# Optimization experiments

Hardware: AMD Instinct MI355X
Metric: run time of the kernel (lower is better)

Reference implementation:

```python
import jax, jax.numpy as jnp
from jax import lax
import numpy as np

H, HKV, D = 16, 4, 128          # query heads, kv heads, head dim
ROT_DIM = 128                    # rotary applied to full head dim
BASE = 10000.0


def rope_cos_sin(S, dtype):
    inv_freq = 1.0 / (BASE ** (jnp.arange(0, ROT_DIM, 2, dtype=jnp.float32) / ROT_DIM))
    t = jnp.arange(S, dtype=jnp.float32)
    freqs = jnp.outer(t, inv_freq)          # (S, ROT_DIM//2)
    return jnp.cos(freqs).astype(dtype), jnp.sin(freqs).astype(dtype)


def apply_rope(x, cos, sin):
    # x: (B, S, h, D); non-interleaved (GPT-NeoX) halves
    d2 = ROT_DIM // 2
    x1, x2 = x[..., :d2], x[..., d2:ROT_DIM]
    c = cos[None, :, None, :]
    s = sin[None, :, None, :]
    rot = jnp.concatenate([x1 * c - x2 * s, x2 * c + x1 * s], axis=-1)
    if ROT_DIM < x.shape[-1]:
        rot = jnp.concatenate([rot, x[..., ROT_DIM:]], axis=-1)
    return rot


def setup_inputs() -> dict:
    key = jax.random.key(0)
    ks = jax.random.split(key, 7)
    B, S, E = 2, 2048, 2048
    qkv_dim = D * (H + 2 * HKV)  # 3072
    return {
        "x": jax.random.normal(ks[0], (B, S, E), jnp.float32),
        "w_in": jax.random.normal(ks[1], (qkv_dim, E), jnp.float32) * (1.0 / np.sqrt(E)),
        "b_in": jax.random.normal(ks[2], (qkv_dim,), jnp.float32) * 0.02,
        "conv_w": jax.random.normal(ks[3], (qkv_dim, 1, 4), jnp.float32) * 0.5,
        "conv_b": jax.random.normal(ks[4], (qkv_dim,), jnp.float32) * 0.02,
        "w_out": jax.random.normal(ks[5], (E, H * D), jnp.float32) * (1.0 / np.sqrt(H * D)),
        "b_out": jax.random.normal(ks[6], (E,), jnp.float32) * 0.02,
    }


def reference(x, w_in, b_in, conv_w, conv_b, w_out, b_out):
    B, S, E = x.shape
    K = conv_w.shape[-1]
    # fused QKV projection
    qkv = x @ w_in.T + b_in                                  # (B, S, 3072)
    # causal depthwise conv1d (torch conv with padding=K-1 then keep first S)
    lhs = jnp.pad(qkv.transpose(0, 2, 1), ((0, 0), (0, 0), (K - 1, 0)))  # (B, C, S+K-1)
    conv = lax.conv_general_dilated(
        lhs, conv_w, (1,), "VALID",
        dimension_numbers=("NCH", "OIH", "NCH"),
        feature_group_count=conv_w.shape[0],
    )
    qkv = (conv + conv_b[None, :, None]).transpose(0, 2, 1)  # (B, S, 3072)
    # split q / kv (GQA)
    q = qkv[..., : H * D].reshape(B, S, H, D)
    kv = qkv[..., H * D :].reshape(B, S, 2, HKV, D)
    cos, sin = rope_cos_sin(S, x.dtype)
    q = apply_rope(q, cos, sin)
    k = apply_rope(kv[:, :, 0], cos, sin)
    v = kv[:, :, 1]
    rep = H // HKV
    k = jnp.repeat(k, rep, axis=2)                           # (B, S, H, D)
    v = jnp.repeat(v, rep, axis=2)
    scale = 1.0 / np.sqrt(D)  # softmax_scale=None -> 1/sqrt(head_dim)
    scores = jnp.einsum("bshd,bthd->bhst", q, k) * scale     # (B, H, S, S)
    causal_mask = jnp.tril(jnp.ones((S, S), bool))
    scores = jnp.where(causal_mask[None, None], scores, jnp.finfo(scores.dtype).min)
    attn = jax.nn.softmax(scores, axis=-1)
    ctx = jnp.einsum("bhst,bthd->bshd", attn, v).reshape(B, S, H * D)
    return ctx @ w_out.T + b_out
```

## Files before the change

### kernel.cpp

```cpp
#include <hip/hip_runtime.h>
#include <type_traits>

#define S_LEN 2048
#define BATCH 2
#define EDIM  2048
#define NH    16
#define NKV   4
#define HDIM  128
#define QKVD  3072
#define QSCALE 0.12751579107188777f

typedef __attribute__((ext_vector_type(8))) short short8;
typedef __attribute__((ext_vector_type(4))) float f32x4;

__device__ __forceinline__ ushort f2bf(float f) {
  union { float f; unsigned u; } un; un.f = f;
  unsigned u = un.u + 0x7fffu + ((un.u >> 16) & 1u);
  return (ushort)(u >> 16);
}
__device__ __forceinline__ float bf2f(ushort h) {
  union { unsigned u; float f; } un; un.u = ((unsigned)h) << 16;
  return un.f;
}
__device__ __forceinline__ unsigned cvt_pk_bf16(float lo, float hi) {
  unsigned r;
  asm("v_cvt_pk_bf16_f32 %0, %1, %2" : "=v"(r) : "v"(lo), "v"(hi));
  return r;
}
__device__ __forceinline__ float fexp2(float x) { return __builtin_amdgcn_exp2f(x); }

__device__ __forceinline__ void load_lds16(const void* g, void* l) {
  __builtin_amdgcn_global_load_lds((const __attribute__((address_space(1))) void*)g,
                                   (__attribute__((address_space(3))) void*)l,
                                   16, 0, 0);
}

__global__ __launch_bounds__(256) void cast3(const float* __restrict__ a,
                                             const float* __restrict__ b,
                                             const float* __restrict__ c,
                                             ushort* __restrict__ oa,
                                             ushort* __restrict__ ob,
                                             ushort* __restrict__ oc) {
  int i = blockIdx.x * 256 + threadIdx.x;
  const float* s; ushort* d; int j;
  if (i < 2097152)      { s = a; d = oa; j = i; }
  else if (i < 3670016) { s = b; d = ob; j = i - 2097152; }
  else                  { s = c; d = oc; j = i - 3670016; }
  float4 v = ((const float4*)s)[j];
  ushort4 o;
  o.x = f2bf(v.x); o.y = f2bf(v.y); o.z = f2bf(v.z); o.w = f2bf(v.w);
  ((ushort4*)d)[j] = o;
}

__global__ __launch_bounds__(256) void transpose_cw(const float* __restrict__ cw,
                                                    float* __restrict__ cwT) {
  int i = blockIdx.x * 256 + threadIdx.x;
  int c = i >> 2, j = i & 3;
  cwT[j * QKVD + c] = cw[i];
}

__global__ __launch_bounds__(256) void rope_table(float* __restrict__ cosT,
                                                  float* __restrict__ sinT) {
  int i = blockIdx.x * 256 + threadIdx.x;
  int s = i >> 6, d = i & 63;
  float inv = expf(-(float)d * 0.14391156831212787f);
  float f = (float)s * inv;
  float sv, cv;
  sincosf(f, &sv, &cv);
  cosT[i] = cv;
  sinT[i] = sv;
}

template <bool OBF>
__global__ __launch_bounds__(256) void gemm_bt(
    const ushort* __restrict__ A, const ushort* __restrict__ Bt,
    const float* __restrict__ bias, void* __restrict__ Cv,
    int M, int N, int K) {
  __shared__ __align__(16) ushort As[128 * 32];
  __shared__ __align__(16) ushort Bs[128 * 32];
  const int tid = threadIdx.x;
  const int wid = tid >> 6, lane = tid & 63;
  const int l15 = lane & 15, lg = lane >> 4;
  const int nTn = N >> 7;
  const int cpx = gridDim.x >> 3;
  const int swz = ((int)blockIdx.x & 7) * cpx + ((int)blockIdx.x >> 3);
  const int m0 = (swz / nTn) * 128, n0 = (swz % nTn) * 128;
  const int wr = (wid >> 1) * 64, wc = (wid & 1) * 64;
  f32x4 acc[4][4] = {};

  for (int k0 = 0; k0 < K; k0 += 32) {
#pragma unroll
    for (int j = 0; j < 2; ++j) {
      const int c = j * 256 + wid * 64 + lane;
      load_lds16(A + (size_t)(m0 + (c >> 2)) * K + k0 + (c & 3) * 8,
                 As + (j * 256 + wid * 64) * 8);
      load_lds16(Bt + (size_t)(n0 + (c >> 2)) * K + k0 + (c & 3) * 8,
                 Bs + (j * 256 + wid * 64) * 8);
    }
    __syncthreads();
    short8 af[4], bf[4];
#pragma unroll
    for (int i = 0; i < 4; i++) {
      af[i] = *(const short8*)&As[(wr + i * 16 + l15) * 32 + lg * 8];
      bf[i] = *(const short8*)&Bs[(wc + i * 16 + l15) * 32 + lg * 8];
    }
#pragma unroll
    for (int mi = 0; mi < 4; mi++)
#pragma unroll
      for (int ni = 0; ni < 4; ni++)
        acc[mi][ni] = __builtin_amdgcn_mfma_f32_16x16x32_bf16(af[mi], bf[ni], acc[mi][ni], 0, 0, 0);
    __syncthreads();
  }

#pragma unroll
  for (int mi = 0; mi < 4; mi++) {
#pragma unroll
    for (int ni = 0; ni < 4; ni++) {
      const int col = n0 + wc + ni * 16 + l15;
      const float bv = bias[col];
#pragma unroll
      for (int r = 0; r < 4; r++) {
        const int row = m0 + wr + mi * 16 + lg * 4 + r;
        if constexpr (OBF)
          ((ushort*)Cv)[(size_t)row * N + col] = f2bf(acc[mi][ni][r] + bv);
        else
          ((float*)Cv)[(size_t)row * N + col] = acc[mi][ni][r] + bv;
      }
    }
  }
}

template <bool OBF>
__global__ __launch_bounds__(512, 2) void gemm256(
    const ushort* __restrict__ A, const ushort* __restrict__ Bt,
    const float* __restrict__ bias, void* __restrict__ Cv,
    int M, int N, int K) {
  __shared__ __align__(16) ushort LA[4][8192];
  __shared__ __align__(16) ushort LB[4][8192];
  const int tid = threadIdx.x;
  const int wid = tid >> 6, lane = tid & 63;
  const int l15 = lane & 15, lg = lane >> 4;
  const int wr = wid >> 2, wc = wid & 3;
  const int nTn = N >> 8;
  const int cpx = gridDim.x >> 3;
  const int swz = ((int)blockIdx.x & 7) * cpx + ((int)blockIdx.x >> 3);
  const int m0 = (swz / nTn) * 256, n0 = (swz % nTn) * 256;
  const ushort* Ag = A + (size_t)m0 * K;
  const ushort* Bg = Bt + (size_t)n0 * K;
  const int coff = (lg ^ ((l15 >> 1) & 3)) * 8;
  const int abase = (wr * 128 + l15) * 32 + coff;
  const int bbase = (wc * 64 + l15) * 32 + coff;
  const int nk = K >> 5;

  f32x4 acc[8][4] = {};

  auto stage_one = [&](const ushort* G, ushort* Ls, int k0) {
#pragma unroll
    for (int i = 0; i < 2; ++i) {
      const int c = i * 512 + tid;
      const int row = c >> 2, cc = c & 3;
      const int scc = cc ^ ((row >> 1) & 3);
      load_lds16(G + (size_t)row * K + k0 + scc * 8,
                 Ls + (i * 512 + wid * 64) * 8);
    }
  };

#pragma unroll
  for (int t = 0; t < 3; ++t) {
    stage_one(Ag, LA[t], t * 32);
    stage_one(Bg, LB[t], t * 32);
  }
  asm volatile("s_waitcnt vmcnt(8)" ::: "memory");
  __builtin_amdgcn_s_barrier();

  auto ktile = [&](auto VMC, auto STG, int t) {
    constexpr int VM = decltype(VMC)::value;
    constexpr bool STAGE = decltype(STG)::value;
    const int slot = t & 3;
    const ushort* Las = LA[slot];
    const ushort* Lbs = LB[slot];
    short8 afr[8], bfr[4];
#pragma unroll
    for (int n = 0; n < 4; ++n) bfr[n] = *(const short8*)&Lbs[bbase + n * 512];
#pragma unroll
    for (int m = 0; m < 8; ++m) afr[m] = *(const short8*)&Las[abase + m * 512];
    if constexpr (STAGE) {
      stage_one(Ag, LA[(t + 3) & 3], (t + 3) * 32);
      stage_one(Bg, LB[(t + 3) & 3], (t + 3) * 32);
    }
    __builtin_amdgcn_s_barrier();
    __builtin_amdgcn_s_setprio(1);
#pragma unroll
    for (int m = 0; m < 8; ++m)
#pragma unroll
      for (int n = 0; n < 4; ++n)
        acc[m][n] = __builtin_amdgcn_mfma_f32_16x16x32_bf16(afr[m], bfr[n], acc[m][n], 0, 0, 0);
    __builtin_amdgcn_s_setprio(0);
    if constexpr (VM == 8)      asm volatile("s_waitcnt vmcnt(8)" ::: "memory");
    else if constexpr (VM == 4) asm volatile("s_waitcnt vmcnt(4)" ::: "memory");
    else if constexpr (VM == 0) asm volatile("s_waitcnt vmcnt(0)" ::: "memory");
    __builtin_amdgcn_s_barrier();
  };

  using tru = std::integral_constant<bool, true>;
  using fal = std::integral_constant<bool, false>;
  for (int t = 0; t + 3 < nk; ++t)
    ktile(std::integral_constant<int, 8>{}, tru{}, t);
  ktile(std::integral_constant<int, 4>{}, fal{}, nk - 3);
  ktile(std::integral_constant<int, 0>{}, fal{}, nk - 2);
  ktile(std::integral_constant<int, -1>{}, fal{}, nk - 1);

#pragma unroll
  for (int m = 0; m < 8; ++m)
#pragma unroll
    for (int n = 0; n < 4; ++n) {
      const int col = n0 + wc * 64 + n * 16 + l15;
      const float bv = bias[col];
#pragma unroll
      for (int r = 0; r < 4; ++r) {
        const int row = m0 + wr * 128 + m * 16 + lg * 4 + r;
        if constexpr (OBF)
          ((ushort*)Cv)[(size_t)row * N + col] = f2bf(acc[m][n][r] + bv);
        else
          ((float*)Cv)[(size_t)row * N + col] = acc[m][n][r] + bv;
      }
    }
}

__global__ __launch_bounds__(256) void conv_rope(
    const ushort* __restrict__ qkv, const float* __restrict__ cwT,
    const float* __restrict__ cb, const float* __restrict__ cosT,
    const float* __restrict__ sinT, ushort* __restrict__ Qo,
    ushort* __restrict__ Ko, ushort* __restrict__ Vo) {
  const int token = blockIdx.x;
  const int s = token & (S_LEN - 1);
  const int p = blockIdx.y * 256 + threadIdx.x;

  auto conv4 = [&](int c0, float out[4]) {
    const float4 bb = *(const float4*)&cb[c0];
    out[0] = bb.x; out[1] = bb.y; out[2] = bb.z; out[3] = bb.w;
#pragma unroll
    for (int j = 0; j < 4; j++) {
      int ss = s - 3 + j;
      if (ss >= 0) {
        ushort4 v = *(const ushort4*)&qkv[(size_t)(token - 3 + j) * QKVD + c0];
        const float4 w = *(const float4*)&cwT[j * QKVD + c0];
        out[0] += bf2f(v.x) * w.x;
        out[1] += bf2f(v.y) * w.y;
        out[2] += bf2f(v.z) * w.z;
        out[3] += bf2f(v.w) * w.w;
      }
    }
  };

  if (p < 256) {
    const int h = p >> 4, d0 = (p & 15) * 4;
    const int c1 = h * 128 + d0;
    float x1[4], x2[4];
    conv4(c1, x1); conv4(c1 + 64, x2);
    const float4 co = *(const float4*)&cosT[s * 64 + d0];
    const float4 si = *(const float4*)&sinT[s * 64 + d0];
    ushort4 o1, o2v;
    o1.x = f2bf((x1[0] * co.x - x2[0] * si.x) * QSCALE);
    o1.y = f2bf((x1[1] * co.y - x2[1] * si.y) * QSCALE);
    o1.z = f2bf((x1[2] * co.z - x2[2] * si.z) * QSCALE);
    o1.w = f2bf((x1[3] * co.w - x2[3] * si.w) * QSCALE);
    o2v.x = f2bf((x2[0] * co.x + x1[0] * si.x) * QSCALE);
    o2v.y = f2bf((x2[1] * co.y + x1[1] * si.y) * QSCALE);
    o2v.z = f2bf((x2[2] * co.z + x1[2] * si.z) * QSCALE);
    o2v.w = f2bf((x2[3] * co.w + x1[3] * si.w) * QSCALE);
    const size_t base = ((size_t)token * NH + h) * HDIM + d0;
    *(ushort4*)&Qo[base] = o1;
    *(ushort4*)&Qo[base + 64] = o2v;
  } else if (p < 320) {
    const int idx = p - 256, h = idx >> 4, d0 = (idx & 15) * 4;
    const int c1 = 2048 + h * 128 + d0;
    float x1[4], x2[4];
    conv4(c1, x1); conv4(c1 + 64, x2);
    const float4 co = *(const float4*)&cosT[s * 64 + d0];
    const float4 si = *(const float4*)&sinT[s * 64 + d0];
    ushort4 o1, o2v;
    o1.x = f2bf(x1[0] * co.x - x2[0] * si.x);
    o1.y = f2bf(x1[1] * co.y - x2[1] * si.y);
    o1.z = f2bf(x1[2] * co.z - x2[2] * si.z);
    o1.w = f2bf(x1[3] * co.w - x2[3] * si.w);
    o2v.x = f2bf(x2[0] * co.x + x1[0] * si.x);
    o2v.y = f2bf(x2[1] * co.y + x1[1] * si.y);
    o2v.z = f2bf(x2[2] * co.z + x1[2] * si.z);
    o2v.w = f2bf(x2[3] * co.w + x1[3] * si.w);
    const size_t base = ((size_t)token * NKV + h) * HDIM + d0;
    *(ushort4*)&Ko[base] = o1;
    *(ushort4*)&Ko[base + 64] = o2v;
  } else if (p < 448) {
    const int idx = p - 320;
    const int c0 = 2560 + idx * 4;
    float v[4];
    conv4(c0, v);
    const int hd = idx * 4;
    const int h = hd >> 7, d = hd & 127;
    ushort4 o;
    o.x = f2bf(v[0]); o.y = f2bf(v[1]); o.z = f2bf(v[2]); o.w = f2bf(v[3]);
    *(ushort4*)&Vo[((size_t)token * NKV + h) * HDIM + d] = o;
  }
}

__global__ __launch_bounds__(256) void transpose_v(const ushort* __restrict__ Vb,
                                                   ushort* __restrict__ Vt) {
  __shared__ ushort t[64][65];
  const int tid = threadIdx.x;
  const int s0 = blockIdx.x * 64, d0 = blockIdx.y * 64;
  const int g = blockIdx.z;
  const int b = g >> 2, kvh = g & 3;
#pragma unroll
  for (int p = 0; p < 8; p++) {
    int idx = p * 256 + tid;
    int r = idx >> 5, c2 = (idx & 31) * 2;
    ushort2 v = *(const ushort2*)&Vb[((size_t)(b * S_LEN + s0 + r) * NKV + kvh) * HDIM + d0 + c2];
    t[r][c2] = v.x; t[r][c2 + 1] = v.y;
  }
  __syncthreads();
#pragma unroll
  for (int p = 0; p < 8; p++) {
    int idx = p * 256 + tid;
    int dr = idx >> 5, sc2 = (idx & 31) * 2;
    ushort2 v; v.x = t[sc2][dr]; v.y = t[sc2 + 1][dr];
    *(ushort2*)&Vt[((size_t)g * HDIM + d0 + dr) * S_LEN + s0 + sc2] = v;
  }
}

__global__ __launch_bounds__(256, 2) void attn(
    const ushort* __restrict__ Q, const ushort* __restrict__ K,
    const ushort* __restrict__ Vt, ushort* __restrict__ ctx) {
  __shared__ __align__(16) ushort Ks[2][64 * 128];
  __shared__ __align__(16) ushort Vs[2][128 * 64];
  const int tid = threadIdx.x;
  const int wid = tid >> 6, lane = tid & 63;
  const int l15 = lane & 15, lg = lane >> 4;
  const int bkv = blockIdx.x;
  const int b = bkv >> 2, kvh = bkv & 3;
  const int h = kvh * 4 + wid;
  const int qb = (gridDim.y - 1) - blockIdx.y;
  const int q0 = qb * 16;

  const ushort* Kbase  = K  + ((size_t)b * S_LEN * NKV + kvh) * HDIM;
  const ushort* Vtbase = Vt + (size_t)bkv * HDIM * S_LEN;

  short8 qf[4];
#pragma unroll
  for (int kd = 0; kd < 4; kd++)
    qf[kd] = *(const short8*)&Q[(((size_t)(b * S_LEN + q0 + l15)) * NH + h) * HDIM + kd * 32 + lg * 8];

  auto stage = [&](int tile, int bufi) {
    const int j0t = tile * 64;
#pragma unroll
    for (int p = 0; p < 4; ++p) {
      const int i = wid * 4 + p;
      {
        const int row = i * 4 + (lane >> 4);
        const int cs  = (lane & 15) ^ (row & 7);
        load_lds16(Kbase + (size_t)(j0t + row) * (NKV * HDIM) + cs * 8,
                   &Ks[bufi][i * 512]);
      }
      {
        const int d  = i * 8 + (lane >> 3);
        const int cs = (lane & 7) ^ (d & 7);
        load_lds16(Vtbase + (size_t)d * S_LEN + j0t + cs * 8,
                   &Vs[bufi][i * 512]);
      }
    }
  };

  f32x4 o2[8] = {};
  float m_run = -3e30f, l_run = 0.f;
  const int ntile = q0 / 64 + 1;
  const int qrow = q0 + l15;

  stage(0, 0);
  __syncthreads();
  int buf = 0;
  for (int jt = 0; jt < ntile; ++jt) {
    const int j0 = jt * 64;
    if (jt + 1 < ntile) stage(jt + 1, buf ^ 1);

    f32x4 sa[4] = {};
#pragma unroll
    for (int t = 0; t < 4; ++t) {
      const int r = t * 16 + l15;
#pragma unroll
      for (int kd = 0; kd < 4; ++kd) {
        short8 kf = *(const short8*)&Ks[buf][r * 128 + (((kd * 4 + lg) ^ (r & 7)) * 8)];
        sa[t] = __builtin_amdgcn_mfma_f32_16x16x32_bf16(kf, qf[kd], sa[t], 0, 0, 0);
      }
    }

    float pv[4][4];
    float mx = -3e30f;
#pragma unroll
    for (int t = 0; t < 4; ++t)
#pragma unroll
      for (int r = 0; r < 4; ++r) {
        float v = sa[t][r];
        if (j0 + t * 16 + lg * 4 + r > qrow) v = -3e30f;
        pv[t][r] = v;
        mx = fmaxf(mx, v);
      }
    mx = fmaxf(mx, __shfl_xor(mx, 16));
    mx = fmaxf(mx, __shfl_xor(mx, 32));
    const float mnew = fmaxf(m_run, mx);
    float sum = 0.f;
#pragma unroll
    for (int t = 0; t < 4; ++t)
#pragma unroll
      for (int r = 0; r < 4; ++r) {
        float p = fexp2(pv[t][r] - mnew);
        pv[t][r] = p;
        sum += p;
      }
    sum += __shfl_xor(sum, 16);
    sum += __shfl_xor(sum, 32);
    const float fac = fexp2(m_run - mnew);
    m_run = mnew;
    l_run = l_run * fac + sum;
#pragma unroll
    for (int dt = 0; dt < 8; ++dt)
#pragma unroll
      for (int r = 0; r < 4; ++r) o2[dt][r] *= fac;

    unsigned pk[4][2];
#pragma unroll
    for (int t = 0; t < 4; ++t)
#pragma unroll
      for (int p = 0; p < 2; ++p)
        pk[t][p] = cvt_pk_bf16(pv[t][2 * p], pv[t][2 * p + 1]);

    union U8 { unsigned u[4]; short8 s; } pfk[2];
#pragma unroll
    for (int ks = 0; ks < 2; ++ks)
#pragma unroll
      for (int j = 0; j < 4; ++j) {
        const int src = ((lg & 1) * 2 + (j >> 1)) * 16 + l15;
        unsigned v0 = __shfl((int)pk[ks * 2][j & 1], src);
        unsigned v1 = __shfl((int)pk[ks * 2 + 1][j & 1], src);
        pfk[ks].u[j] = (lg >= 2) ? v1 : v0;
      }

#pragma unroll
    for (int dt = 0; dt < 8; ++dt) {
      const int d = dt * 16 + l15;
#pragma unroll
      for (int ks = 0; ks < 2; ++ks) {
        short8 vf = *(const short8*)&Vs[buf][d * 64 + (((ks * 4 + lg) ^ (d & 7)) * 8)];
        o2[dt] = __builtin_amdgcn_mfma_f32_16x16x32_bf16(vf, pfk[ks].s, o2[dt], 0, 0, 0);
      }
    }

    __syncthreads();
    buf ^= 1;
  }

  const float inv_l = 1.f / l_run;
  const size_t obase = (((size_t)(b * S_LEN + q0 + l15)) * NH + h) * HDIM;
#pragma unroll
  for (int dt = 0; dt < 8; ++dt) {
    ushort4 w;
    w.x = f2bf(o2[dt][0] * inv_l);
    w.y = f2bf(o2[dt][1] * inv_l);
    w.z = f2bf(o2[dt][2] * inv_l);
    w.w = f2bf(o2[dt][3] * inv_l);
    *(ushort4*)&ctx[obase + dt * 16 + lg * 4] = w;
  }
}

extern "C" void kernel_launch(void* const* d_in, const int* in_sizes, int n_in,
                              void* d_out, int out_size, void* d_ws, size_t ws_size,
                              hipStream_t stream) {
  const float* x      = (const float*)d_in[0];
  const float* w_in   = (const float*)d_in[1];
  const float* b_in   = (const float*)d_in[2];
  const float* conv_w = (const float*)d_in[3];
  const float* conv_b = (const float*)d_in[4];
  const float* w_out  = (const float*)d_in[5];
  const float* b_out  = (const float*)d_in[6];
  float* out = (float*)d_out;

  char* ws = (char*)d_ws;
  size_t off = 0;
  ushort* xbf  = (ushort*)(ws + off); off += (size_t)4096 * 2048 * 2;
  ushort* wibf = (ushort*)(ws + off); off += (size_t)3072 * 2048 * 2;
  ushort* wobf = (ushort*)(ws + off); off += (size_t)2048 * 2048 * 2;
  ushort* qkv  = (ushort*)(ws + off); off += (size_t)4096 * 3072 * 2;
  ushort* Qb   = (ushort*)(ws + off); off += (size_t)4096 * 16 * 128 * 2;
  ushort* Kb   = (ushort*)(ws + off); off += (size_t)4096 * 4 * 128 * 2;
  ushort* Vb   = (ushort*)(ws + off); off += (size_t)4096 * 4 * 128 * 2;
  float*  cosT = (float*)(ws + off);  off += (size_t)2048 * 64 * 4;
  float*  sinT = (float*)(ws + off);  off += (size_t)2048 * 64 * 4;
  float*  cwT  = (float*)(ws + off);  off += (size_t)4 * QKVD * 4;
  ushort* Vtb  = (ushort*)qkv;

  cast3<<<18432, 256, 0, stream>>>(x, w_in, w_out, xbf, wibf, wobf);
  transpose_cw<<<48, 256, 0, stream>>>(conv_w, cwT);
  rope_table<<<512, 256, 0, stream>>>(cosT, sinT);

  gemm256<true><<<192, 512, 0, stream>>>(xbf, wibf, b_in, qkv, 4096, 3072, 2048);
  conv_rope<<<dim3(4096, 2), 256, 0, stream>>>(qkv, cwT, conv_b, cosT, sinT, Qb, Kb, Vb);
  transpose_v<<<dim3(32, 2, 8), 256, 0, stream>>>(Vb, Vtb);
  attn<<<dim3(8, 128), 256, 0, stream>>>(Qb, Kb, Vtb, xbf);
  gemm_bt<false><<<512, 256, 0, stream>>>(xbf, wobf, b_out, out, 4096, 2048, 2048);
}
```

Baseline: 230.7 us.

## Process two 16-row query tiles per attention block to reuse staged K/V

Each attention block now handles 32 query rows (two 16-row sub-tiles per wave) instead of 16, so every K/V tile staged into LDS feeds twice the MFMA work. The grid's y dimension is halved to match. This cuts K/V global-to-LDS traffic and barrier count per query row. In exchange it doubles the accumulator and Q-fragment registers, which may lower occupancy under launch_bounds(256,2), and leaves fewer blocks for the causal load balance.

Result: no change. 235.2 us (+2.0%).

```diff
diff --git a/kernel.cpp b/kernel.cpp
--- a/kernel.cpp
+++ b/kernel.cpp
@@ -340,15 +340,17 @@
   const int b = bkv >> 2, kvh = bkv & 3;
   const int h = kvh * 4 + wid;
   const int qb = (gridDim.y - 1) - blockIdx.y;
-  const int q0 = qb * 16;
+  const int q0 = qb * 32;
 
   const ushort* Kbase  = K  + ((size_t)b * S_LEN * NKV + kvh) * HDIM;
   const ushort* Vtbase = Vt + (size_t)bkv * HDIM * S_LEN;
 
-  short8 qf[4];
-#pragma unroll
-  for (int kd = 0; kd < 4; kd++)
-    qf[kd] = *(const short8*)&Q[(((size_t)(b * S_LEN + q0 + l15)) * NH + h) * HDIM + kd * 32 + lg * 8];
+  short8 qfA[4], qfB[4];
+#pragma unroll
+  for (int kd = 0; kd < 4; kd++) {
+    qfA[kd] = *(const short8*)&Q[(((size_t)(b * S_LEN + q0 + l15)) * NH + h) * HDIM + kd * 32 + lg * 8];
+    qfB[kd] = *(const short8*)&Q[(((size_t)(b * S_LEN + q0 + 16 + l15)) * NH + h) * HDIM + kd * 32 + lg * 8];
+  }
 
   auto stage = [&](int tile, int bufi) {
     const int j0t = tile * 64;
@@ -370,10 +372,84 @@
     }
   };
 
-  f32x4 o2[8] = {};
-  float m_run = -3e30f, l_run = 0.f;
-  const int ntile = q0 / 64 + 1;
-  const int qrow = q0 + l15;
+  f32x4 oA[8] = {}, oB[8] = {};
+  float mA = -3e30f, lA = 0.f, mB = -3e30f, lB = 0.f;
+  const int ntile = (q0 + 31) / 64 + 1;
+
+  auto process = [&](const short8 (&qfX)[4], f32x4 (&oX)[8], float &mX, float &lX,
+                     int qrow, int j0, int bufi) {
+    f32x4 sa[4] = {};
+#pragma unroll
+    for (int t = 0; t < 4; ++t) {
+      const int r = t * 16 + l15;
+#pragma unroll
+      for (int kd = 0; kd < 4; ++kd) {
+        short8 kf = *(const short8*)&Ks[bufi][r * 128 + (((kd * 4 + lg) ^ (r & 7)) * 8)];
+        sa[t] = __builtin_amdgcn_mfma_f32_16x16x32_bf16(kf, qfX[kd], sa[t], 0, 0, 0);
+      }
+    }
+
+    float pv[4][4];
+    float mx = -3e30f;
+#pragma unroll
+    for (int t = 0; t < 4; ++t)
+#pragma unroll
+      for (int r = 0; r < 4; ++r) {
+        float v = sa[t][r];
+        if (j0 + t * 16 + lg * 4 + r > qrow) v = -3e30f;
+        pv[t][r] = v;
+        mx = fmaxf(mx, v);
+      }
+    mx = fmaxf(mx, __shfl_xor(mx, 16));
+    mx = fmaxf(mx, __shfl_xor(mx, 32));
+    const float mnew = fmaxf(mX, mx);
+    float sum = 0.f;
+#pragma unroll
+    for (int t = 0; t < 4; ++t)
+#pragma unroll
+      for (int r = 0; r < 4; ++r) {
+        float p = fexp2(pv[t][r] - mnew);
+        pv[t][r] = p;
+        sum += p;
+      }
+    sum += __shfl_xor(sum, 16);
+    sum += __shfl_xor(sum, 32);
+    const float fac = fexp2(mX - mnew);
+    mX = mnew;
+    lX = lX * fac + sum;
+#pragma unroll
+    for (int dt = 0; dt < 8; ++dt)
+#pragma unroll
+      for (int r = 0; r < 4; ++r) oX[dt][r] *= fac;
+
+    unsigned pk[4][2];
+#pragma unroll
+    for (int t = 0; t < 4; ++t)
+#pragma unroll
+      for (int p = 0; p < 2; ++p)
+        pk[t][p] = cvt_pk_bf16(pv[t][2 * p], pv[t][2 * p + 1]);
+
+    union U8 { unsigned u[4]; short8 s; } pfk[2];
+#pragma unroll
+    for (int ks = 0; ks < 2; ++ks)
+#pragma unroll
+      for (int j = 0; j < 4; ++j) {
+        const int src = ((lg & 1) * 2 + (j >> 1)) * 16 + l15;
+        unsigned v0 = __shfl((int)pk[ks * 2][j & 1], src);
+        unsigned v1 = __shfl((int)pk[ks * 2 + 1][j & 1], src);
+        pfk[ks].u[j] = (lg >= 2) ? v1 : v0;
+      }
+
+#pragma unroll
+    for (int dt = 0; dt < 8; ++dt) {
+      const int d = dt * 16 + l15;
+#pragma unroll
+      for (int ks = 0; ks < 2; ++ks) {
+        short8 vf = *(const short8*)&Vs[bufi][d * 64 + (((ks * 4 + lg) ^ (d & 7)) * 8)];
+        oX[dt] = __builtin_amdgcn_mfma_f32_16x16x32_bf16(vf, pfk[ks].s, oX[dt], 0, 0, 0);
+      }
+    }
+  };
 
   stage(0, 0);
   __syncthreads();
@@ -382,92 +458,38 @@
     const int j0 = jt * 64;
     if (jt + 1 < ntile) stage(jt + 1, buf ^ 1);
 
-    f32x4 sa[4] = {};
-#pragma unroll
-    for (int t = 0; t < 4; ++t) {
-      const int r = t * 16 + l15;
-#pragma unroll
-      for (int kd = 0; kd < 4; ++kd) {
-        short8 kf = *(const short8*)&Ks[buf][r * 128 + (((kd * 4 + lg) ^ (r & 7)) * 8)];
-        sa[t] = __builtin_amdgcn_mfma_f32_16x16x32_bf16(kf, qf[kd], sa[t], 0, 0, 0);
-      }
-    }
-
-    float pv[4][4];
-    float mx = -3e30f;
-#pragma unroll
-    for (int t = 0; t < 4; ++t)
-#pragma unroll
-      for (int r = 0; r < 4; ++r) {
-        float v = sa[t][r];
-        if (j0 + t * 16 + lg * 4 + r > qrow) v = -3e30f;
-        pv[t][r] = v;
-        mx = fmaxf(mx, v);
-      }
-    mx = fmaxf(mx, __shfl_xor(mx, 16));
-    mx = fmaxf(mx, __shfl_xor(mx, 32));
-    const float mnew = fmaxf(m_run, mx);
-    float sum = 0.f;
-#pragma unroll
-    for (int t = 0; t < 4; ++t)
-#pragma unroll
-      for (int r = 0; r < 4; ++r) {
-        float p = fexp2(pv[t][r] - mnew);
-        pv[t][r] = p;
-        sum += p;
-      }
-    sum += __shfl_xor(sum, 16);
-    sum += __shfl_xor(sum, 32);
-    const float fac = fexp2(m_run - mnew);
-    m_run = mnew;
-    l_run = l_run * fac + sum;
-#pragma unroll
-    for (int dt = 0; dt < 8; ++dt)
-#pragma unroll
-      for (int r = 0; r < 4; ++r) o2[dt][r] *= fac;
-
-    unsigned pk[4][2];
-#pragma unroll
-    for (int t = 0; t < 4; ++t)
-#pragma unroll
-      for (int p = 0; p < 2; ++p)
-        pk[t][p] = cvt_pk_bf16(pv[t][2 * p], pv[t][2 * p + 1]);
-
-    union U8 { unsigned u[4]; short8 s; } pfk[2];
-#pragma unroll
-    for (int ks = 0; ks < 2; ++ks)
-#pragma unroll
-      for (int j = 0; j < 4; ++j) {
-        const int src = ((lg & 1) * 2 + (j >> 1)) * 16 + l15;
-        unsigned v0 = __shfl((int)pk[ks * 2][j & 1], src);
-        unsigned v1 = __shfl((int)pk[ks * 2 + 1][j & 1], src);
-        pfk[ks].u[j] = (lg >= 2) ? v1 : v0;
-      }
-
-#pragma unroll
-    for (int dt = 0; dt < 8; ++dt) {
-      const int d = dt * 16 + l15;
-#pragma unroll
-      for (int ks = 0; ks < 2; ++ks) {
-        short8 vf = *(const short8*)&Vs[buf][d * 64 + (((ks * 4 + lg) ^ (d & 7)) * 8)];
-        o2[dt] = __builtin_amdgcn_mfma_f32_16x16x32_bf16(vf, pfk[ks].s, o2[dt], 0, 0, 0);
-      }
-    }
+    process(qfA, oA, mA, lA, q0 + l15, j0, buf);
+    process(qfB, oB, mB, lB, q0 + 16 + l15, j0, buf);
 
     __syncthreads();
     buf ^= 1;
   }
 
-  const float inv_l = 1.f / l_run;
-  const size_t obase = (((size_t)(b * S_LEN + q0 + l15)) * NH + h) * HDIM;
-#pragma unroll
-  for (int dt = 0; dt < 8; ++dt) {
-    ushort4 w;
-    w.x = f2bf(o2[dt][0] * inv_l);
-    w.y = f2bf(o2[dt][1] * inv_l);
-    w.z = f2bf(o2[dt][2] * inv_l);
-    w.w = f2bf(o2[dt][3] * inv_l);
-    *(ushort4*)&ctx[obase + dt * 16 + lg * 4] = w;
+  {
+    const float inv_l = 1.f / lA;
+    const size_t obase = (((size_t)(b * S_LEN + q0 + l15)) * NH + h) * HDIM;
+#pragma unroll
+    for (int dt = 0; dt < 8; ++dt) {
+      ushort4 w;
+      w.x = f2bf(oA[dt][0] * inv_l);
+      w.y = f2bf(oA[dt][1] * inv_l);
+      w.z = f2bf(oA[dt][2] * inv_l);
+      w.w = f2bf(oA[dt][3] * inv_l);
+      *(ushort4*)&ctx[obase + dt * 16 + lg * 4] = w;
+    }
+  }
+  {
+    const float inv_l = 1.f / lB;
+    const size_t obase = (((size_t)(b * S_LEN + q0 + 16 + l15)) * NH + h) * HDIM;
+#pragma unroll
+    for (int dt = 0; dt < 8; ++dt) {
+      ushort4 w;
+      w.x = f2bf(oB[dt][0] * inv_l);
+      w.y = f2bf(oB[dt][1] * inv_l);
+      w.z = f2bf(oB[dt][2] * inv_l);
+      w.w = f2bf(oB[dt][3] * inv_l);
+      *(ushort4*)&ctx[obase + dt * 16 + lg * 4] = w;
+    }
   }
 }
 
@@ -504,6 +526,6 @@
   gemm256<true><<<192, 512, 0, stream>>>(xbf, wibf, b_in, qkv, 4096, 3072, 2048);
   conv_rope<<<dim3(4096, 2), 256, 0, stream>>>(qkv, cwT, conv_b, cosT, sinT, Qb, Kb, Vb);
   transpose_v<<<dim3(32, 2, 8), 256, 0, stream>>>(Vb, Vtb);
-  attn<<<dim3(8, 128), 256, 0, stream>>>(Qb, Kb, Vtb, xbf);
+  attn<<<dim3(8, 64), 256, 0, stream>>>(Qb, Kb, Vtb, xbf);
   gemm_bt<false><<<512, 256, 0, stream>>>(xbf, wobf, b_out, out, 4096, 2048, 2048);
 }
```
